# Performance work log

Hardware: AMD Instinct MI355X
Metric: run time of the kernel (lower is better)

The kernel has to match this reference:

```python
import jax, jax.numpy as jnp
import numpy as np

THRESHOLD = 0.0  # default float threshold, non-learned path
SURROGATE_TAU = 0.1

@jax.custom_vjp
def jumprelu(x):
    # Forward: hard threshold x * 1[x > THRESHOLD]
    return x * (x > THRESHOLD).astype(x.dtype)

def _jumprelu_fwd(x):
    return jumprelu(x), x

def _jumprelu_bwd(x, g):
    # Smooth surrogate gradient of x * sigmoid(x/tau)
    tau = SURROGATE_TAU
    sig = jax.nn.sigmoid(x / tau)
    surrogate = sig + x * sig * (1.0 - sig) / tau
    return (g * surrogate,)

jumprelu.defvjp(_jumprelu_fwd, _jumprelu_bwd)

NUM_TRANSFORMS = 64
D_MODEL = 2048
RANK = 32
BATCH = 2048

def setup_inputs() -> dict:
    key = jax.random.key(0)
    kx, kv, ku, ke = jax.random.split(key, 4)
    scale = (1.0 / (D_MODEL * RANK)) ** 0.25
    x = jax.random.normal(kx, (BATCH, D_MODEL), dtype=jnp.float32)
    V = jax.random.normal(kv, (NUM_TRANSFORMS, RANK, D_MODEL), dtype=jnp.float32) * scale
    U = jax.random.normal(ku, (NUM_TRANSFORMS, D_MODEL, RANK), dtype=jnp.float32) * scale
    encoder = jax.random.normal(ke, (NUM_TRANSFORMS, D_MODEL), dtype=jnp.float32)
    encoder = encoder / jnp.linalg.norm(encoder, axis=1, keepdims=True)
    bias = jnp.full((NUM_TRANSFORMS,), -1.0, dtype=jnp.float32)
    return {"x": x, "V": V, "U": U, "encoder": encoder, "bias": bias}

def reference(x, V, U, encoder, bias):
    # pre_acts: (batch, num_transforms)
    pre_acts = x @ encoder.T - bias
    gate = jumprelu(pre_acts)
    # Vx: (n, b, r); UVx: (n, b, d)
    Vx = jnp.einsum('nrd,bd->nbr', V, x)
    UVx = jnp.einsum('ndr,nbr->nbd', U, Vx)
    gated = UVx * gate.T[:, :, None]
    output = gated.sum(axis=0)  # (batch, d_model)
    u_norms = jnp.linalg.norm(U.reshape(U.shape[0], -1), axis=1)
    v_norms = jnp.linalg.norm(V.reshape(V.shape[0], -1), axis=1)
    frobenius_norms = u_norms * v_norms / (D_MODEL * RANK) ** 0.5
    return (output, gate, frobenius_norms)
```

## Files before the change

### kernel.cpp

```cpp
#include <hip/hip_runtime.h>


#define D_MODEL 2048
#define BATCH   2048
#define NT      64
#define RANK    32

typedef __attribute__((ext_vector_type(8))) __bf16 bf16x8;
typedef __attribute__((ext_vector_type(4))) float  f32x4;
typedef __attribute__((ext_vector_type(8))) unsigned short ushort8;

__device__ __forceinline__ unsigned short f2bf(float f) {
  unsigned int u = __builtin_bit_cast(unsigned int, f);
  u += 0x7FFFu + ((u >> 16) & 1u);
  return (unsigned short)(u >> 16);
}

__device__ __forceinline__ void gload_lds16(const void* g, void* l) {
  __builtin_amdgcn_global_load_lds(
      (const __attribute__((address_space(1))) unsigned int*)g,
      (__attribute__((address_space(3))) unsigned int*)l,
      16, 0, 0);
}

template <int N>
__device__ __forceinline__ void vm_wait_barrier() {
  if constexpr (N == 0)
    asm volatile("s_waitcnt vmcnt(0)\ns_barrier" ::: "memory");
  else if constexpr (N == 8)
    asm volatile("s_waitcnt vmcnt(8)\ns_barrier" ::: "memory");
  else if constexpr (N == 12)
    asm volatile("s_waitcnt vmcnt(12)\ns_barrier" ::: "memory");
  else
    static_assert(N == 0 || N == 8 || N == 12, "add vmcnt case");
}


__device__ __forceinline__ void block_reduce_store(float ss, float* dst, int slot) {
  __shared__ float red[256];
  int t = threadIdx.x;
  red[t] = ss;
  __syncthreads();
  for (int s = 128; s > 0; s >>= 1) {
    if (t < s) red[t] += red[t + s];
    __syncthreads();
  }
  if (t == 0) dst[slot] = red[0];
}

__global__ void k_prep(const float4* __restrict__ x, const float4* __restrict__ enc,
                       const float4* __restrict__ V, const float4* __restrict__ U,
                       ushort4* __restrict__ xb, ushort4* __restrict__ encb,
                       ushort4* __restrict__ Vb, unsigned short* __restrict__ Ut,
                       float* __restrict__ partV, float* __restrict__ partU) {
  int bid = blockIdx.x, t = threadIdx.x;
  if (bid < 1024) {
#pragma unroll
    for (int it = 0; it < 4; ++it) {
      int i = bid * 1024 + it * 256 + t;
      float4 v = x[i];
      ushort4 o;
      o.x = f2bf(v.x); o.y = f2bf(v.y); o.z = f2bf(v.z); o.w = f2bf(v.w);
      xb[i] = o;
    }
  } else if (bid < 1152) {
    int i = (bid - 1024) * 256 + t;
    float4 v = enc[i];
    ushort4 o;
    o.x = f2bf(v.x); o.y = f2bf(v.y); o.z = f2bf(v.z); o.w = f2bf(v.w);
    encb[i] = o;
  } else if (bid < 1408) {
    int b = bid - 1152;
    size_t base4 = (size_t)b * 4096;
    float ss = 0.f;
    for (int it = 0; it < 16; ++it) {
      size_t idx = base4 + t + it * 256;
      float4 v = V[idx];
      ss += v.x * v.x + v.y * v.y + v.z * v.z + v.w * v.w;
      ushort4 o;
      o.x = f2bf(v.x); o.y = f2bf(v.y); o.z = f2bf(v.z); o.w = f2bf(v.w);
      Vb[idx] = o;
    }
    block_reduce_store(ss, partV, b);
  } else {
    int b = bid - 1408;
    int n = b >> 2;
    size_t base4 = (size_t)b * 4096;
    float ss = 0.f;
    for (int it = 0; it < 8; ++it) {
      size_t i2 = (size_t)(it * 256 + t) * 2;
      size_t idx4 = base4 + i2;
      float4 v0 = U[idx4];
      float4 v1 = U[idx4 + 1];
      ss += v0.x * v0.x + v0.y * v0.y + v0.z * v0.z + v0.w * v0.w;
      ss += v1.x * v1.x + v1.y * v1.y + v1.z * v1.z + v1.w * v1.w;
      size_t e = idx4 * 4 - (size_t)n * (D_MODEL * RANK);
      int dcol = (int)(e >> 5);
      int r = (int)(e & 31);
      ushort8 o;
      o[0] = f2bf(v0.x); o[1] = f2bf(v0.y); o[2] = f2bf(v0.z); o[3] = f2bf(v0.w);
      o[4] = f2bf(v1.x); o[5] = f2bf(v1.y); o[6] = f2bf(v1.z); o[7] = f2bf(v1.w);
      *(ushort8*)(Ut + (size_t)dcol * 2048 + n * 32 + r) = o;
    }
    block_reduce_store(ss, partU, b);
  }
}

__global__ void k_gate_reduce(const float* __restrict__ part, const float* __restrict__ bias,
                              float* __restrict__ gate,
                              const float* __restrict__ pU, const float* __restrict__ pV,
                              float* __restrict__ frob) {
  int t = threadIdx.x;
  if (blockIdx.x == 0 && t < NT) {
    float su = pU[4 * t] + pU[4 * t + 1] + pU[4 * t + 2] + pU[4 * t + 3];
    float sv = pV[4 * t] + pV[4 * t + 1] + pV[4 * t + 2] + pV[4 * t + 3];
    frob[t] = sqrtf(su) * sqrtf(sv) * (1.0f / 256.0f);
  }
#pragma unroll
  for (int u = 0; u < 4; ++u) {
    int idx = blockIdx.x * 1024 + u * 256 + t;
    float s = 0.f;
#pragma unroll
    for (int z = 0; z < 8; ++z) s += part[(size_t)z * (BATCH * NT) + idx];
    float pre = s - bias[idx & (NT - 1)];
    gate[idx] = pre > 0.f ? pre : 0.f;
  }
}

template <int WGM, int WGN, int MI, int NJ, int EPI, int SWZ>
__global__ __launch_bounds__(WGM * WGN * 64, 2)
void gemm_bt(const unsigned short* __restrict__ A,
             const unsigned short* __restrict__ Bt,
             const float* __restrict__ aux,
             unsigned short* __restrict__ outB,
             float* __restrict__ outF, int K, int klen) {
  constexpr int VW = WGM * WGN;
  constexpr int BM = WGM * MI * 16;
  constexpr int BN = WGN * NJ * 16;
  constexpr int BK = 128;
  constexpr int GA = BM / (4 * VW);
  constexpr int GB = BN / (4 * VW);
  constexpr int LPW = GA + GB;
  constexpr int HBUF = (BM + BN) * BK;
  __shared__ __align__(16) unsigned short smem[2 * HBUF];

  const int tid = threadIdx.x;
  const int w = tid >> 6;
  const int lane = tid & 63;
  const int quad = lane >> 4;
  const int l15 = lane & 15;
  const int wm = w % WGM;
  const int wn = w / WGM;

  int blockM, blockN, kbeg;
  if constexpr (SWZ) {
    const int lin = blockIdx.x;
    const int xcd = lin & 7;
    const int i = lin >> 3;
    blockM = (xcd & 3) * 4 + (i & 3);
    blockN = (xcd >> 2) * 8 + (i >> 2);
    kbeg = 0;
  } else {
    blockN = blockIdx.x;
    blockM = blockIdx.y;
    kbeg = blockIdx.z * klen;
  }

  const int lrow4 = lane >> 4;
  const int key = ((w & 3) << 2) | lrow4;
  const int lq = l15 ^ key;
  const unsigned short* Ag = A + (size_t)(blockM * BM + w * 4 + lrow4) * K + kbeg + lq * 8;
  const unsigned short* Bg = Bt + (size_t)(blockN * BN + w * 4 + lrow4) * K + kbeg + lq * 8;

  const int rfA = wm * MI * 16 + l15;
  const int rfB = wn * NJ * 16 + l15;

  f32x4 acc[MI][NJ];
  const f32x4 z = {0.f, 0.f, 0.f, 0.f};
#pragma unroll
  for (int i = 0; i < MI; ++i)
#pragma unroll
    for (int j = 0; j < NJ; ++j) acc[i][j] = z;

  auto stage = [&](int buf, int k0) {
    unsigned short* As = smem + buf * HBUF;
    unsigned short* Bs = As + BM * BK;
#pragma unroll
    for (int j = 0; j < GA; ++j)
      gload_lds16(Ag + (size_t)(j * VW * 4) * K + k0,
                  (char*)As + (j * VW + w) * 1024);
#pragma unroll
    for (int j = 0; j < GB; ++j)
      gload_lds16(Bg + (size_t)(j * VW * 4) * K + k0,
                  (char*)Bs + (j * VW + w) * 1024);
  };

  stage(0, 0);

  const int nt = klen / BK;
  int cur = 0;
  for (int t = 0; t < nt; ++t) {
    if (t + 1 < nt) {
      stage(cur ^ 1, (t + 1) * BK);
      vm_wait_barrier<LPW>();
    } else {
      vm_wait_barrier<0>();
    }
    const unsigned short* As = smem + cur * HBUF;
    const unsigned short* Bs = As + BM * BK;
#pragma unroll
    for (int s = 0; s < 4; ++s) {
      bf16x8 af[MI], bfr[NJ];
#pragma unroll
      for (int i = 0; i < MI; ++i)
        af[i] = *(const bf16x8*)((const char*)As + (rfA + i * 16) * 256 +
                                 (((s * 4 + quad) ^ l15) << 4));
#pragma unroll
      for (int j = 0; j < NJ; ++j)
        bfr[j] = *(const bf16x8*)((const char*)Bs + (rfB + j * 16) * 256 +
                                  (((s * 4 + quad) ^ l15) << 4));
#pragma unroll
      for (int i = 0; i < MI; ++i)
#pragma unroll
        for (int j = 0; j < NJ; ++j)
          acc[i][j] = __builtin_amdgcn_mfma_f32_16x16x32_bf16(af[i], bfr[j], acc[i][j], 0, 0, 0);
    }
    asm volatile("s_barrier" ::: "memory");
    cur ^= 1;
  }

  const int row0 = blockM * BM + wm * MI * 16 + quad * 4;
  const int col0 = blockN * BN + wn * NJ * 16 + l15;
#pragma unroll
  for (int i = 0; i < MI; ++i) {
#pragma unroll
    for (int j = 0; j < NJ; ++j) {
      const int col = col0 + j * 16;
#pragma unroll
      for (int t = 0; t < 4; ++t) {
        const int row = row0 + i * 16 + t;
        float v = acc[i][j][t];
        if constexpr (EPI == 0) {
          float g = aux[(size_t)row * NT + (col >> 5)];
          outB[(size_t)row * 2048 + col] = f2bf(v * g);
        } else if constexpr (EPI == 1) {
          outF[(size_t)row * 2048 + col] = v;
        } else {
          outF[(size_t)blockIdx.z * (BATCH * NT) + (size_t)row * NT + col] = v;
        }
      }
    }
  }
}


extern "C" void kernel_launch(void* const* d_in, const int* in_sizes, int n_in,
                              void* d_out, int out_size, void* d_ws, size_t ws_size,
                              hipStream_t stream) {
  const float* x    = (const float*)d_in[0];
  const float* V    = (const float*)d_in[1];
  const float* U    = (const float*)d_in[2];
  const float* enc  = (const float*)d_in[3];
  const float* bias = (const float*)d_in[4];

  float* out  = (float*)d_out;
  float* gate = out + (size_t)BATCH * D_MODEL;
  float* frob = gate + (size_t)BATCH * NT;

  char* ws = (char*)d_ws;
  unsigned short* xb   = (unsigned short*)(ws);
  unsigned short* Vb   = (unsigned short*)(ws + (8u << 20));
  unsigned short* Ut   = (unsigned short*)(ws + (16u << 20));
  unsigned short* Yg   = (unsigned short*)(ws + (24u << 20));
  float* gatePart      = (float*)Yg;
  unsigned short* encb = (unsigned short*)(ws + (32u << 20));
  float* partU = (float*)(ws + (32u << 20) + 262144);
  float* partV = partU + 256;

  k_prep<<<1664, 256, 0, stream>>>((const float4*)x, (const float4*)enc,
                                   (const float4*)V, (const float4*)U,
                                   (ushort4*)xb, (ushort4*)encb, (ushort4*)Vb, Ut,
                                   partV, partU);

  gemm_bt<4, 1, 2, 4, 3, 0><<<dim3(1, 16, 8), 256, 0, stream>>>(
      xb, encb, nullptr, nullptr, gatePart, D_MODEL, 256);
  k_gate_reduce<<<128, 256, 0, stream>>>(gatePart, bias, gate, partU, partV, frob);

  gemm_bt<2, 4, 4, 2, 0, 1><<<dim3(256, 1, 1), 512, 0, stream>>>(
      xb, Vb, gate, Yg, nullptr, D_MODEL, D_MODEL);

  gemm_bt<2, 4, 4, 2, 1, 1><<<dim3(256, 1, 1), 512, 0, stream>>>(
      Yg, Ut, nullptr, nullptr, out, D_MODEL, D_MODEL);
}
```

Before: 149.7 us.

## Fuse gate GEMM and gate reduction into the V-projection GEMM

Removes the split-K gate GEMM and the separate gate-reduce kernel. Each V-projection block now also loads its 4 encoder rows into LDS each K-step and accumulates the pre-activations with extra MFMAs, one wave column per encoder slice. The partial sums are combined through LDS in the epilogue, then bias and ReLU are applied, and the result gates the bf16 output directly. This saves two launches and the partial-sum round trip through global memory, at the cost of extra MFMAs, an extra LDS load per stage, and an epilogue barrier in the main GEMM.

```diff
diff --git a/kernel.cpp b/kernel.cpp
--- a/kernel.cpp
+++ b/kernel.cpp
@@ -29,10 +29,10 @@
     asm volatile("s_waitcnt vmcnt(0)\ns_barrier" ::: "memory");
   else if constexpr (N == 8)
     asm volatile("s_waitcnt vmcnt(8)\ns_barrier" ::: "memory");
-  else if constexpr (N == 12)
-    asm volatile("s_waitcnt vmcnt(12)\ns_barrier" ::: "memory");
+  else if constexpr (N == 9)
+    asm volatile("s_waitcnt vmcnt(9)\ns_barrier" ::: "memory");
   else
-    static_assert(N == 0 || N == 8 || N == 12, "add vmcnt case");
+    static_assert(N == 0 || N == 8 || N == 9, "add vmcnt case");
 }
 
 
@@ -106,43 +106,28 @@
   }
 }
 
-__global__ void k_gate_reduce(const float* __restrict__ part, const float* __restrict__ bias,
-                              float* __restrict__ gate,
-                              const float* __restrict__ pU, const float* __restrict__ pV,
-                              float* __restrict__ frob) {
-  int t = threadIdx.x;
-  if (blockIdx.x == 0 && t < NT) {
-    float su = pU[4 * t] + pU[4 * t + 1] + pU[4 * t + 2] + pU[4 * t + 3];
-    float sv = pV[4 * t] + pV[4 * t + 1] + pV[4 * t + 2] + pV[4 * t + 3];
-    frob[t] = sqrtf(su) * sqrtf(sv) * (1.0f / 256.0f);
-  }
-#pragma unroll
-  for (int u = 0; u < 4; ++u) {
-    int idx = blockIdx.x * 1024 + u * 256 + t;
-    float s = 0.f;
-#pragma unroll
-    for (int z = 0; z < 8; ++z) s += part[(size_t)z * (BATCH * NT) + idx];
-    float pre = s - bias[idx & (NT - 1)];
-    gate[idx] = pre > 0.f ? pre : 0.f;
-  }
-}
-
 template <int WGM, int WGN, int MI, int NJ, int EPI, int SWZ>
 __global__ __launch_bounds__(WGM * WGN * 64, 2)
 void gemm_bt(const unsigned short* __restrict__ A,
              const unsigned short* __restrict__ Bt,
-             const float* __restrict__ aux,
              unsigned short* __restrict__ outB,
-             float* __restrict__ outF, int K, int klen) {
+             float* __restrict__ outF, int K, int klen,
+             const unsigned short* __restrict__ Eb,
+             const float* __restrict__ bias,
+             const float* __restrict__ pU, const float* __restrict__ pV,
+             float* __restrict__ frob, float* __restrict__ gateOut) {
   constexpr int VW = WGM * WGN;
   constexpr int BM = WGM * MI * 16;
   constexpr int BN = WGN * NJ * 16;
   constexpr int BK = 128;
   constexpr int GA = BM / (4 * VW);
   constexpr int GB = BN / (4 * VW);
-  constexpr int LPW = GA + GB;
+  constexpr int LPW = GA + GB + (EPI == 0 ? 1 : 0);
   constexpr int HBUF = (BM + BN) * BK;
-  __shared__ __align__(16) unsigned short smem[2 * HBUF];
+  constexpr int ENCS = (EPI == 0) ? 512 : 0;
+  static_assert(EPI != 0 || (WGM == 2 && WGN == 4 && MI == 4 && NJ == 2),
+                "EPI0 fused-gate layout requires 2x4 waves, MI=4, NJ=2");
+  __shared__ __align__(16) unsigned short smem[2 * HBUF + 2 * ENCS];
 
   const int tid = threadIdx.x;
   const int w = tid >> 6;
@@ -152,35 +137,46 @@
   const int wm = w % WGM;
   const int wn = w / WGM;
 
-  int blockM, blockN, kbeg;
+  int blockM, blockN;
   if constexpr (SWZ) {
     const int lin = blockIdx.x;
     const int xcd = lin & 7;
     const int i = lin >> 3;
     blockM = (xcd & 3) * 4 + (i & 3);
     blockN = (xcd >> 2) * 8 + (i >> 2);
-    kbeg = 0;
   } else {
     blockN = blockIdx.x;
     blockM = blockIdx.y;
-    kbeg = blockIdx.z * klen;
+  }
+
+  if constexpr (EPI == 0) {
+    if (blockIdx.x == 0 && tid < NT) {
+      float su = pU[4 * tid] + pU[4 * tid + 1] + pU[4 * tid + 2] + pU[4 * tid + 3];
+      float sv = pV[4 * tid] + pV[4 * tid + 1] + pV[4 * tid + 2] + pV[4 * tid + 3];
+      frob[tid] = sqrtf(su) * sqrtf(sv) * (1.0f / 256.0f);
+    }
   }
 
   const int lrow4 = lane >> 4;
   const int key = ((w & 3) << 2) | lrow4;
   const int lq = l15 ^ key;
-  const unsigned short* Ag = A + (size_t)(blockM * BM + w * 4 + lrow4) * K + kbeg + lq * 8;
-  const unsigned short* Bg = Bt + (size_t)(blockN * BN + w * 4 + lrow4) * K + kbeg + lq * 8;
+  const unsigned short* Ag = A + (size_t)(blockM * BM + w * 4 + lrow4) * K + lq * 8;
+  const unsigned short* Bg = Bt + (size_t)(blockN * BN + w * 4 + lrow4) * K + lq * 8;
+  const unsigned short* Eg = (EPI == 0)
+      ? Eb + (size_t)(blockN * 4 + lrow4) * K + l15 * 8 : nullptr;
 
   const int rfA = wm * MI * 16 + l15;
   const int rfB = wn * NJ * 16 + l15;
 
   f32x4 acc[MI][NJ];
+  f32x4 acc_g[MI];
   const f32x4 z = {0.f, 0.f, 0.f, 0.f};
 #pragma unroll
-  for (int i = 0; i < MI; ++i)
+  for (int i = 0; i < MI; ++i) {
+    acc_g[i] = z;
 #pragma unroll
     for (int j = 0; j < NJ; ++j) acc[i][j] = z;
+  }
 
   auto stage = [&](int buf, int k0) {
     unsigned short* As = smem + buf * HBUF;
@@ -193,6 +189,8 @@
     for (int j = 0; j < GB; ++j)
       gload_lds16(Bg + (size_t)(j * VW * 4) * K + k0,
                   (char*)Bs + (j * VW + w) * 1024);
+    if constexpr (EPI == 0)
+      gload_lds16(Eg + k0, (char*)(smem + 2 * HBUF + buf * ENCS));
   };
 
   stage(0, 0);
@@ -208,6 +206,7 @@
     }
     const unsigned short* As = smem + cur * HBUF;
     const unsigned short* Bs = As + BM * BK;
+    const unsigned short* Es = smem + 2 * HBUF + cur * ENCS;
 #pragma unroll
     for (int s = 0; s < 4; ++s) {
       bf16x8 af[MI], bfr[NJ];
@@ -219,6 +218,15 @@
       for (int j = 0; j < NJ; ++j)
         bfr[j] = *(const bf16x8*)((const char*)Bs + (rfB + j * 16) * 256 +
                                   (((s * 4 + quad) ^ l15) << 4));
+      if constexpr (EPI == 0) {
+        if (s == wn) {
+          bf16x8 be = *(const bf16x8*)((const char*)Es +
+                                       ((l15 & 3) * 128 + s * 32 + quad * 8) * 2);
+#pragma unroll
+          for (int i = 0; i < MI; ++i)
+            acc_g[i] = __builtin_amdgcn_mfma_f32_16x16x32_bf16(af[i], be, acc_g[i], 0, 0, 0);
+        }
+      }
 #pragma unroll
       for (int i = 0; i < MI; ++i)
 #pragma unroll
@@ -231,22 +239,45 @@
 
   const int row0 = blockM * BM + wm * MI * 16 + quad * 4;
   const int col0 = blockN * BN + wn * NJ * 16 + l15;
-#pragma unroll
-  for (int i = 0; i < MI; ++i) {
-#pragma unroll
-    for (int j = 0; j < NJ; ++j) {
-      const int col = col0 + j * 16;
+  if constexpr (EPI == 0) {
+    float* tmp = (float*)smem;
+    if (l15 < 4) {
+#pragma unroll
+      for (int i = 0; i < MI; ++i)
+#pragma unroll
+        for (int r = 0; r < 4; ++r)
+          tmp[(((wn * 2 + wm) * MI + i) * 16 + quad * 4 + r) * 4 + l15] = acc_g[i][r];
+    }
+    __syncthreads();
+    const float bv = bias[blockN * 4 + wn];
+#pragma unroll
+    for (int i = 0; i < MI; ++i) {
 #pragma unroll
       for (int t = 0; t < 4; ++t) {
+        float s0 = tmp[(((0 * 2 + wm) * MI + i) * 16 + quad * 4 + t) * 4 + wn]
+                 + tmp[(((1 * 2 + wm) * MI + i) * 16 + quad * 4 + t) * 4 + wn]
+                 + tmp[(((2 * 2 + wm) * MI + i) * 16 + quad * 4 + t) * 4 + wn]
+                 + tmp[(((3 * 2 + wm) * MI + i) * 16 + quad * 4 + t) * 4 + wn];
+        float pre = s0 - bv;
+        float g = pre > 0.f ? pre : 0.f;
         const int row = row0 + i * 16 + t;
-        float v = acc[i][j][t];
-        if constexpr (EPI == 0) {
-          float g = aux[(size_t)row * NT + (col >> 5)];
-          outB[(size_t)row * 2048 + col] = f2bf(v * g);
-        } else if constexpr (EPI == 1) {
-          outF[(size_t)row * 2048 + col] = v;
-        } else {
-          outF[(size_t)blockIdx.z * (BATCH * NT) + (size_t)row * NT + col] = v;
+        if (l15 == 0)
+          gateOut[(size_t)row * NT + blockN * 4 + wn] = g;
+#pragma unroll
+        for (int j = 0; j < NJ; ++j)
+          outB[(size_t)row * 2048 + col0 + j * 16] = f2bf(acc[i][j][t] * g);
+      }
+    }
+  } else {
+#pragma unroll
+    for (int i = 0; i < MI; ++i) {
+#pragma unroll
+      for (int j = 0; j < NJ; ++j) {
+        const int col = col0 + j * 16;
+#pragma unroll
+        for (int t = 0; t < 4; ++t) {
+          const int row = row0 + i * 16 + t;
+          outF[(size_t)row * 2048 + col] = acc[i][j][t];
         }
       }
     }
@@ -272,7 +303,6 @@
   unsigned short* Vb   = (unsigned short*)(ws + (8u << 20));
   unsigned short* Ut   = (unsigned short*)(ws + (16u << 20));
   unsigned short* Yg   = (unsigned short*)(ws + (24u << 20));
-  float* gatePart      = (float*)Yg;
   unsigned short* encb = (unsigned short*)(ws + (32u << 20));
   float* partU = (float*)(ws + (32u << 20) + 262144);
   float* partV = partU + 256;
@@ -282,13 +312,11 @@
                                    (ushort4*)xb, (ushort4*)encb, (ushort4*)Vb, Ut,
                                    partV, partU);
 
-  gemm_bt<4, 1, 2, 4, 3, 0><<<dim3(1, 16, 8), 256, 0, stream>>>(
-      xb, encb, nullptr, nullptr, gatePart, D_MODEL, 256);
-  k_gate_reduce<<<128, 256, 0, stream>>>(gatePart, bias, gate, partU, partV, frob);
-
   gemm_bt<2, 4, 4, 2, 0, 1><<<dim3(256, 1, 1), 512, 0, stream>>>(
-      xb, Vb, gate, Yg, nullptr, D_MODEL, D_MODEL);
+      xb, Vb, Yg, nullptr, D_MODEL, D_MODEL,
+      encb, bias, partU, partV, frob, gate);
 
   gemm_bt<2, 4, 4, 2, 1, 1><<<dim3(256, 1, 1), 512, 0, stream>>>(
-      Yg, Ut, nullptr, nullptr, out, D_MODEL, D_MODEL);
-}
+      Yg, Ut, nullptr, out, D_MODEL, D_MODEL,
+      nullptr, nullptr, nullptr, nullptr, nullptr, nullptr);
+}
```

Result: faster. 145.5 us (median of 2 runs) (-2.8%).
